# Performance work log

Measured on AMD Instinct MI355X. Metric: run time of the kernel, lower is better.

Reference implementation:

```python
import jax, jax.numpy as jnp
import numpy as np

H, F, E = 1024, 2816, 8   # hidden_size, intermediate_size, num_local_experts
B, S = 2, 2048
TOP_K = 2


def setup_inputs() -> dict:
    key = jax.random.key(0)
    ks = jax.random.split(key, 5)
    scale = 0.02
    return {
        "hidden_states": jax.random.normal(ks[0], (B, S, H), jnp.float32),
        "gate_w": jax.random.normal(ks[1], (E, H), jnp.float32) * scale,
        "w1": jax.random.normal(ks[2], (E, F, H), jnp.float32) * scale,
        "w3": jax.random.normal(ks[3], (E, F, H), jnp.float32) * scale,
        "w2": jax.random.normal(ks[4], (E, H, F), jnp.float32) * scale,
    }


def reference(hidden_states, gate_w, w1, w3, w2):
    b, s, h = hidden_states.shape
    e = gate_w.shape[0]
    T = b * s
    x = hidden_states.reshape(T, h)                      # [T, H]
    router_logits = x @ gate_w.T                         # [T, E]
    probs = jax.nn.softmax(router_logits, axis=-1)
    topw, sel = jax.lax.top_k(probs, TOP_K)              # [T, K]
    topw = topw / jnp.sum(topw, axis=-1, keepdims=True)  # renormalize over top-k
    # dense combine weights [T, E] (equivalent to the per-expert scatter/index_add)
    comb = jnp.zeros((T, e), x.dtype).at[jnp.arange(T)[:, None], sel].add(topw)
    hidden = jax.nn.silu(jnp.einsum('th,efh->etf', x, w1)) * jnp.einsum('th,efh->etf', x, w3)
    y = jnp.einsum('etf,ehf->eth', hidden, w2)           # [E, T, H]
    out = jnp.einsum('eth,te->th', y, comb)              # weighted scatter-combine
    return out.reshape(b, s, h), router_logits
```

## Files before the change

### kernel.cpp

```cpp
#include <hip/hip_runtime.h>
#include <hip/hip_bf16.h>
#include <stdint.h>

#define T_TOK 4096
#define H_DIM 1024
#define F_DIM 2816
#define E_NUM 8

typedef __attribute__((ext_vector_type(8))) __bf16 bf16x8;
typedef __attribute__((ext_vector_type(4))) float floatx4;
typedef __attribute__((address_space(3))) char lds_char;
typedef __attribute__((address_space(1))) const char glb_char;

__device__ __forceinline__ void gload16(const void* g, void* l) {
  __builtin_amdgcn_global_load_lds((glb_char*)g, (lds_char*)l, 16, 0, 0);
}

__device__ __forceinline__ unsigned pack2bf16(float a, float b) {
  unsigned ua = __builtin_bit_cast(unsigned, a);
  unsigned ub = __builtin_bit_cast(unsigned, b);
  ua += 0x7fffu + ((ua >> 16) & 1u);
  ub += 0x7fffu + ((ub >> 16) & 1u);
  return (ua >> 16) | (ub & 0xffff0000u);
}

__device__ __forceinline__ int swz(int row, int colb) {
  return (row * 128 + colb) ^ ((row & 7) << 4);
}

__global__ __launch_bounds__(256) void convert_kernel(
    const float* __restrict__ src, __hip_bfloat16* __restrict__ dst,
    int nchunk8) {
  int i = blockIdx.x * blockDim.x + threadIdx.x;
  const int stride = gridDim.x * blockDim.x;
  for (; i < nchunk8; i += stride) {
    const float4* s = (const float4*)(src + (size_t)i * 8);
    float4 a = s[0], b = s[1];
    uint4 p;
    p.x = pack2bf16(a.x, a.y); p.y = pack2bf16(a.z, a.w);
    p.z = pack2bf16(b.x, b.y); p.w = pack2bf16(b.z, b.w);
    *(uint4*)((char*)dst + (size_t)i * 16) = p;
  }
}

__global__ __launch_bounds__(256) void router_kernel(
    const float* __restrict__ x, const float* __restrict__ gate,
    float* __restrict__ logits_out, __hip_bfloat16* __restrict__ xb,
    int* __restrict__ counts, int* __restrict__ idx_list,
    float* __restrict__ wgt_list)
{
  const int wv = threadIdx.x >> 6;
  const int lane = threadIdx.x & 63;
  const int t = blockIdx.x * 4 + wv;

  const float4* xr = (const float4*)(x + (size_t)t * H_DIM);
  const float4* g4 = (const float4*)gate;

  float acc[E_NUM];
#pragma unroll
  for (int e = 0; e < E_NUM; ++e) acc[e] = 0.f;

  unsigned* xbo = (unsigned*)(xb + (size_t)t * H_DIM);
#pragma unroll
  for (int j = 0; j < 4; ++j) {
    int i = j * 64 + lane;
    float4 xv = xr[i];
    uint2 pk;
    pk.x = pack2bf16(xv.x, xv.y);
    pk.y = pack2bf16(xv.z, xv.w);
    *(uint2*)(xbo + i * 2) = pk;
#pragma unroll
    for (int e = 0; e < E_NUM; ++e) {
      float4 gv = g4[e * 256 + i];
      acc[e] += xv.x * gv.x + xv.y * gv.y + xv.z * gv.z + xv.w * gv.w;
    }
  }
#pragma unroll
  for (int off = 32; off > 0; off >>= 1) {
#pragma unroll
    for (int e = 0; e < E_NUM; ++e) acc[e] += __shfl_xor(acc[e], off, 64);
  }

  if (lane == 0) {
#pragma unroll
    for (int e = 0; e < E_NUM; ++e) logits_out[(size_t)t * E_NUM + e] = acc[e];
    int i0 = 0; float v0 = acc[0];
#pragma unroll
    for (int e = 1; e < E_NUM; ++e) if (acc[e] > v0) { v0 = acc[e]; i0 = e; }
    int i1 = -1; float v1 = -1e30f;
#pragma unroll
    for (int e = 0; e < E_NUM; ++e)
      if (e != i0 && acc[e] > v1) { v1 = acc[e]; i1 = e; }
    float p1 = __expf(v1 - v0);
    float w0 = 1.f / (1.f + p1);
    float w1 = p1 / (1.f + p1);
    int pos0 = atomicAdd(&counts[i0], 1);
    idx_list[i0 * T_TOK + pos0] = t;
    wgt_list[i0 * T_TOK + pos0] = w0;
    int pos1 = atomicAdd(&counts[i1], 1);
    idx_list[i1 * T_TOK + pos1] = t;
    wgt_list[i1 * T_TOK + pos1] = w1;
  }
}

__global__ void scan_kernel(const int* __restrict__ counts,
                            int* __restrict__ offsets) {
  if (threadIdx.x == 0) {
    int s = 0;
    for (int e = 0; e < E_NUM; ++e) { offsets[e] = s; s += counts[e]; }
  }
}

__global__ __launch_bounds__(256) void gemm1_kernel(
    const __hip_bfloat16* __restrict__ xb,
    const __hip_bfloat16* __restrict__ w1b,
    const __hip_bfloat16* __restrict__ w3b,
    const int* __restrict__ counts, const int* __restrict__ offsets,
    const int* __restrict__ idx_list, __hip_bfloat16* __restrict__ hidden)
{
  const int e = blockIdx.z;
  const int n_e = counts[e];
  const int tm = blockIdx.y;
  if (n_e == 0 || tm * 128 >= n_e) return;
  const int tn = blockIdx.x;
  const int f0 = tn * 128;
  const int off_e = offsets[e];

  __shared__ char sA[16384];
  __shared__ char sB1[16384];
  __shared__ char sB3[16384];

  const int tid = threadIdx.x;
  const int lane = tid & 63;
  const int wv = tid >> 6;
  const int wrow = (wv >> 1) * 64;
  const int wcol = (wv & 1) * 64;
  const int csw = ((lane & 7) ^ (lane >> 3)) * 16;
  const int rsub = lane >> 3;

  const char* xbp = (const char*)xb;
  size_t arow[4];
#pragma unroll
  for (int i = 0; i < 4; ++i) {
    int r = wv * 32 + i * 8 + rsub;
    int pos = tm * 128 + r;
    int p = pos < n_e ? pos : n_e - 1;
    arow[i] = (size_t)idx_list[e * T_TOK + p] * (H_DIM * 2);
  }
  const char* w1p = (const char*)w1b + ((size_t)e * F_DIM + f0) * (H_DIM * 2);
  const char* w3p = (const char*)w3b + ((size_t)e * F_DIM + f0) * (H_DIM * 2);

  floatx4 acc1[4][4], acc3[4][4];
#pragma unroll
  for (int m = 0; m < 4; ++m)
#pragma unroll
    for (int n = 0; n < 4; ++n)
#pragma unroll
      for (int r = 0; r < 4; ++r) { acc1[m][n][r] = 0.f; acc3[m][n][r] = 0.f; }

  for (int kt = 0; kt < H_DIM / 64; ++kt) {
    const int kb = kt * 128;
    __syncthreads();
#pragma unroll
    for (int i = 0; i < 4; ++i) {
      int r = wv * 32 + i * 8 + rsub;
      int ldsoff = wv * 4096 + i * 1024;
      gload16(xbp + arow[i] + kb + csw, sA + ldsoff);
      gload16(w1p + (size_t)r * (H_DIM * 2) + kb + csw, sB1 + ldsoff);
      gload16(w3p + (size_t)r * (H_DIM * 2) + kb + csw, sB3 + ldsoff);
    }
    asm volatile("s_waitcnt vmcnt(0)" ::: "memory");
    __syncthreads();
#pragma unroll
    for (int kk = 0; kk < 2; ++kk) {
      const int colb = kk * 64 + (lane >> 4) * 16;
      bf16x8 af[4], bf1[4], bf3[4];
#pragma unroll
      for (int m = 0; m < 4; ++m)
        af[m] = *(const bf16x8*)(sA + swz(wrow + m * 16 + (lane & 15), colb));
#pragma unroll
      for (int n = 0; n < 4; ++n) {
        bf1[n] = *(const bf16x8*)(sB1 + swz(wcol + n * 16 + (lane & 15), colb));
        bf3[n] = *(const bf16x8*)(sB3 + swz(wcol + n * 16 + (lane & 15), colb));
      }
#pragma unroll
      for (int m = 0; m < 4; ++m)
#pragma unroll
        for (int n = 0; n < 4; ++n) {
          acc1[m][n] = __builtin_amdgcn_mfma_f32_16x16x32_bf16(
              af[m], bf1[n], acc1[m][n], 0, 0, 0);
          acc3[m][n] = __builtin_amdgcn_mfma_f32_16x16x32_bf16(
              af[m], bf3[n], acc3[m][n], 0, 0, 0);
        }
    }
  }

#pragma unroll
  for (int m = 0; m < 4; ++m) {
#pragma unroll
    for (int r = 0; r < 4; ++r) {
      int rl = wrow + m * 16 + ((lane >> 4) << 2) + r;
      int pos = tm * 128 + rl;
      if (pos < n_e) {
        __hip_bfloat16* hrow = hidden + (size_t)(off_e + pos) * F_DIM + f0;
#pragma unroll
        for (int n = 0; n < 4; ++n) {
          float h1 = acc1[m][n][r];
          float h3 = acc3[m][n][r];
          float h = (h1 / (1.f + __expf(-h1))) * h3;
          hrow[wcol + n * 16 + (lane & 15)] = __float2bfloat16(h);
        }
      }
    }
  }
}

__global__ __launch_bounds__(256) void gemm2_kernel(
    const __hip_bfloat16* __restrict__ hidden,
    const __hip_bfloat16* __restrict__ w2b,
    const int* __restrict__ counts, const int* __restrict__ offsets,
    const int* __restrict__ idx_list, const float* __restrict__ wgt_list,
    float* __restrict__ out)
{
  const int e = blockIdx.z;
  const int n_e = counts[e];
  const int tm = blockIdx.y;
  if (n_e == 0 || tm * 128 >= n_e) return;
  const int tn = blockIdx.x;
  const int n0 = tn * 128;
  const int off_e = offsets[e];

  __shared__ short sA[128 * 64];
  __shared__ short sB[128 * 64];
  __shared__ int s_tok[128];
  __shared__ float s_wgt[128];

  const int tid = threadIdx.x;
  if (tid < 128) {
    int pos = tm * 128 + tid;
    if (pos < n_e) {
      s_tok[tid] = idx_list[e * T_TOK + pos];
      s_wgt[tid] = wgt_list[e * T_TOK + pos];
    } else {
      s_tok[tid] = -1;
      s_wgt[tid] = 0.f;
    }
  }
  const int lane = tid & 63;
  const int wv = tid >> 6;
  const int wrow = (wv >> 1) * 64;
  const int wcol = (wv & 1) * 64;
  const int cc = tid & 7;
  const int rbase = tid >> 3;

  floatx4 acc[4][4];
#pragma unroll
  for (int m = 0; m < 4; ++m)
#pragma unroll
    for (int n = 0; n < 4; ++n)
#pragma unroll
      for (int r = 0; r < 4; ++r) acc[m][n][r] = 0.f;

  const __hip_bfloat16* w2e = w2b + ((size_t)e * H_DIM + n0) * F_DIM;

  for (int kt = 0; kt < F_DIM / 64; ++kt) {
    const int k0 = kt * 64;
    __syncthreads();
#pragma unroll
    for (int i = 0; i < 4; ++i) {
      int r = rbase + 32 * i;
      int pos = tm * 128 + r;
      int pr = pos < n_e ? pos : n_e - 1;
      uint4 av = *(const uint4*)(hidden + (size_t)(off_e + pr) * F_DIM +
                                 k0 + cc * 8);
      *(uint4*)((char*)sA + swz(r, cc * 16)) = av;
      uint4 bv = *(const uint4*)(w2e + (size_t)r * F_DIM + k0 + cc * 8);
      *(uint4*)((char*)sB + swz(r, cc * 16)) = bv;
    }
    __syncthreads();
#pragma unroll
    for (int kk = 0; kk < 2; ++kk) {
      const int colb = kk * 64 + (lane >> 4) * 16;
      bf16x8 af[4], bf[4];
#pragma unroll
      for (int m = 0; m < 4; ++m)
        af[m] = *(const bf16x8*)((const char*)sA +
                                 swz(wrow + m * 16 + (lane & 15), colb));
#pragma unroll
      for (int n = 0; n < 4; ++n)
        bf[n] = *(const bf16x8*)((const char*)sB +
                                 swz(wcol + n * 16 + (lane & 15), colb));
#pragma unroll
      for (int m = 0; m < 4; ++m)
#pragma unroll
        for (int n = 0; n < 4; ++n)
          acc[m][n] = __builtin_amdgcn_mfma_f32_16x16x32_bf16(
              af[m], bf[n], acc[m][n], 0, 0, 0);
    }
  }

#pragma unroll
  for (int m = 0; m < 4; ++m) {
#pragma unroll
    for (int r = 0; r < 4; ++r) {
      int rl = wrow + m * 16 + ((lane >> 4) << 2) + r;
      int tok = s_tok[rl];
      if (tok >= 0) {
        float wgt = s_wgt[rl];
        float* orow = out + (size_t)tok * H_DIM + n0;
#pragma unroll
        for (int n = 0; n < 4; ++n)
          atomicAdd(&orow[wcol + n * 16 + (lane & 15)], wgt * acc[m][n][r]);
      }
    }
  }
}

__global__ __launch_bounds__(256) void gemm1_fb(
    const __hip_bfloat16* __restrict__ xb,
    const float* __restrict__ w1, const float* __restrict__ w3,
    const int* __restrict__ counts, const int* __restrict__ offsets,
    const int* __restrict__ idx_list, __hip_bfloat16* __restrict__ hidden)
{
  const int e = blockIdx.z;
  const int n_e = counts[e];
  const int tm = blockIdx.y;
  if (n_e == 0 || tm * 128 >= n_e) return;
  const int tn = blockIdx.x;
  const int f0 = tn * 128;
  const int off_e = offsets[e];

  __shared__ short sA[128 * 64];
  __shared__ short sB1[128 * 64];
  __shared__ short sB3[128 * 64];
  __shared__ int s_row[128];

  const int tid = threadIdx.x;
  if (tid < 128) {
    int pos = tm * 128 + tid;
    int p = pos < n_e ? pos : n_e - 1;
    s_row[tid] = idx_list[e * T_TOK + p];
  }
  const int lane = tid & 63;
  const int wv = tid >> 6;
  const int wrow = (wv >> 1) * 64;
  const int wcol = (wv & 1) * 64;
  const int cc = tid & 7;
  const int rbase = tid >> 3;

  floatx4 acc1[4][4], acc3[4][4];
#pragma unroll
  for (int m = 0; m < 4; ++m)
#pragma unroll
    for (int n = 0; n < 4; ++n)
#pragma unroll
      for (int r = 0; r < 4; ++r) { acc1[m][n][r] = 0.f; acc3[m][n][r] = 0.f; }

  const float* w1e = w1 + (size_t)e * F_DIM * H_DIM + (size_t)f0 * H_DIM;
  const float* w3e = w3 + (size_t)e * F_DIM * H_DIM + (size_t)f0 * H_DIM;

  for (int kt = 0; kt < H_DIM / 64; ++kt) {
    const int k0 = kt * 64;
    __syncthreads();
#pragma unroll
    for (int i = 0; i < 4; ++i) {
      int r = rbase + 32 * i;
      uint4 av = *(const uint4*)(xb + (size_t)s_row[r] * H_DIM + k0 + cc * 8);
      *(uint4*)((char*)sA + swz(r, cc * 16)) = av;
      const float4* p1 = (const float4*)(w1e + (size_t)r * H_DIM + k0 + cc * 8);
      float4 a1 = p1[0], b1 = p1[1];
      uint4 pb1;
      pb1.x = pack2bf16(a1.x, a1.y); pb1.y = pack2bf16(a1.z, a1.w);
      pb1.z = pack2bf16(b1.x, b1.y); pb1.w = pack2bf16(b1.z, b1.w);
      *(uint4*)((char*)sB1 + swz(r, cc * 16)) = pb1;
      const float4* p3 = (const float4*)(w3e + (size_t)r * H_DIM + k0 + cc * 8);
      float4 a3 = p3[0], b3 = p3[1];
      uint4 pb3;
      pb3.x = pack2bf16(a3.x, a3.y); pb3.y = pack2bf16(a3.z, a3.w);
      pb3.z = pack2bf16(b3.x, b3.y); pb3.w = pack2bf16(b3.z, b3.w);
      *(uint4*)((char*)sB3 + swz(r, cc * 16)) = pb3;
    }
    __syncthreads();
#pragma unroll
    for (int kk = 0; kk < 2; ++kk) {
      const int colb = kk * 64 + (lane >> 4) * 16;
      bf16x8 af[4], bf1[4], bf3[4];
#pragma unroll
      for (int m = 0; m < 4; ++m)
        af[m] = *(const bf16x8*)((const char*)sA +
                                 swz(wrow + m * 16 + (lane & 15), colb));
#pragma unroll
      for (int n = 0; n < 4; ++n) {
        bf1[n] = *(const bf16x8*)((const char*)sB1 +
                                  swz(wcol + n * 16 + (lane & 15), colb));
        bf3[n] = *(const bf16x8*)((const char*)sB3 +
                                  swz(wcol + n * 16 + (lane & 15), colb));
      }
#pragma unroll
      for (int m = 0; m < 4; ++m)
#pragma unroll
        for (int n = 0; n < 4; ++n) {
          acc1[m][n] = __builtin_amdgcn_mfma_f32_16x16x32_bf16(
              af[m], bf1[n], acc1[m][n], 0, 0, 0);
          acc3[m][n] = __builtin_amdgcn_mfma_f32_16x16x32_bf16(
              af[m], bf3[n], acc3[m][n], 0, 0, 0);
        }
    }
  }
#pragma unroll
  for (int m = 0; m < 4; ++m) {
#pragma unroll
    for (int r = 0; r < 4; ++r) {
      int rl = wrow + m * 16 + ((lane >> 4) << 2) + r;
      int pos = tm * 128 + rl;
      if (pos < n_e) {
        __hip_bfloat16* hrow = hidden + (size_t)(off_e + pos) * F_DIM + f0;
#pragma unroll
        for (int n = 0; n < 4; ++n) {
          float h1 = acc1[m][n][r];
          float h3 = acc3[m][n][r];
          float h = (h1 / (1.f + __expf(-h1))) * h3;
          hrow[wcol + n * 16 + (lane & 15)] = __float2bfloat16(h);
        }
      }
    }
  }
}

__global__ __launch_bounds__(256) void gemm2_fb(
    const __hip_bfloat16* __restrict__ hidden, const float* __restrict__ w2,
    const int* __restrict__ counts, const int* __restrict__ offsets,
    const int* __restrict__ idx_list, const float* __restrict__ wgt_list,
    float* __restrict__ out)
{
  const int e = blockIdx.z;
  const int n_e = counts[e];
  const int tm = blockIdx.y;
  if (n_e == 0 || tm * 128 >= n_e) return;
  const int tn = blockIdx.x;
  const int n0 = tn * 128;
  const int off_e = offsets[e];

  __shared__ short sA[128 * 64];
  __shared__ short sB[128 * 64];
  __shared__ int s_tok[128];
  __shared__ float s_wgt[128];

  const int tid = threadIdx.x;
  if (tid < 128) {
    int pos = tm * 128 + tid;
    if (pos < n_e) {
      s_tok[tid] = idx_list[e * T_TOK + pos];
      s_wgt[tid] = wgt_list[e * T_TOK + pos];
    } else {
      s_tok[tid] = -1;
      s_wgt[tid] = 0.f;
    }
  }
  const int lane = tid & 63;
  const int wv = tid >> 6;
  const int wrow = (wv >> 1) * 64;
  const int wcol = (wv & 1) * 64;
  const int cc = tid & 7;
  const int rbase = tid >> 3;

  floatx4 acc[4][4];
#pragma unroll
  for (int m = 0; m < 4; ++m)
#pragma unroll
    for (int n = 0; n < 4; ++n)
#pragma unroll
      for (int r = 0; r < 4; ++r) acc[m][n][r] = 0.f;

  const float* w2e = w2 + (size_t)e * H_DIM * F_DIM + (size_t)n0 * F_DIM;

  for (int kt = 0; kt < F_DIM / 64; ++kt) {
    const int k0 = kt * 64;
    __syncthreads();
#pragma unroll
    for (int i = 0; i < 4; ++i) {
      int r = rbase + 32 * i;
      int pos = tm * 128 + r;
      int pr = pos < n_e ? pos : n_e - 1;
      uint4 av = *(const uint4*)(hidden + (size_t)(off_e + pr) * F_DIM +
                                 k0 + cc * 8);
      *(uint4*)((char*)sA + swz(r, cc * 16)) = av;
      const float4* pb = (const float4*)(w2e + (size_t)r * F_DIM + k0 + cc * 8);
      float4 ba = pb[0], bb = pb[1];
      uint4 pk;
      pk.x = pack2bf16(ba.x, ba.y); pk.y = pack2bf16(ba.z, ba.w);
      pk.z = pack2bf16(bb.x, bb.y); pk.w = pack2bf16(bb.z, bb.w);
      *(uint4*)((char*)sB + swz(r, cc * 16)) = pk;
    }
    __syncthreads();
#pragma unroll
    for (int kk = 0; kk < 2; ++kk) {
      const int colb = kk * 64 + (lane >> 4) * 16;
      bf16x8 af[4], bf[4];
#pragma unroll
      for (int m = 0; m < 4; ++m)
        af[m] = *(const bf16x8*)((const char*)sA +
                                 swz(wrow + m * 16 + (lane & 15), colb));
#pragma unroll
      for (int n = 0; n < 4; ++n)
        bf[n] = *(const bf16x8*)((const char*)sB +
                                 swz(wcol + n * 16 + (lane & 15), colb));
#pragma unroll
      for (int m = 0; m < 4; ++m)
#pragma unroll
        for (int n = 0; n < 4; ++n)
          acc[m][n] = __builtin_amdgcn_mfma_f32_16x16x32_bf16(
              af[m], bf[n], acc[m][n], 0, 0, 0);
    }
  }
#pragma unroll
  for (int m = 0; m < 4; ++m) {
#pragma unroll
    for (int r = 0; r < 4; ++r) {
      int rl = wrow + m * 16 + ((lane >> 4) << 2) + r;
      int tok = s_tok[rl];
      if (tok >= 0) {
        float wgt = s_wgt[rl];
        float* orow = out + (size_t)tok * H_DIM + n0;
#pragma unroll
        for (int n = 0; n < 4; ++n)
          atomicAdd(&orow[wcol + n * 16 + (lane & 15)], wgt * acc[m][n][r]);
      }
    }
  }
}

extern "C" void kernel_launch(void* const* d_in, const int* in_sizes, int n_in,
                              void* d_out, int out_size, void* d_ws,
                              size_t ws_size, hipStream_t stream) {
  const float* x = (const float*)d_in[0];
  const float* gate = (const float*)d_in[1];
  const float* w1 = (const float*)d_in[2];
  const float* w3 = (const float*)d_in[3];
  const float* w2 = (const float*)d_in[4];

  float* out = (float*)d_out;
  float* logits = out + (size_t)T_TOK * H_DIM;

  char* ws = (char*)d_ws;
  const size_t WEB = (size_t)E_NUM * F_DIM * H_DIM * 2;
  const size_t o_idx = 256;
  const size_t o_wgt = o_idx + (size_t)E_NUM * T_TOK * 4;
  const size_t o_xb  = o_wgt + (size_t)E_NUM * T_TOK * 4;
  const size_t o_hid = o_xb + (size_t)T_TOK * H_DIM * 2;
  const size_t o_w1b = o_hid + (size_t)2 * T_TOK * F_DIM * 2;
  const size_t o_w3b = o_w1b + WEB;
  const size_t o_w2b = o_w3b + WEB;
  const size_t need  = o_w2b + WEB;

  int* counts = (int*)ws;
  int* offsets = counts + 8;
  int* idx_list = (int*)(ws + o_idx);
  float* wgt_list = (float*)(ws + o_wgt);
  __hip_bfloat16* xb = (__hip_bfloat16*)(ws + o_xb);
  __hip_bfloat16* hidden = (__hip_bfloat16*)(ws + o_hid);

  hipMemsetAsync(counts, 0, 64, stream);
  hipMemsetAsync(out, 0, (size_t)T_TOK * H_DIM * sizeof(float), stream);

  if (ws_size >= need) {
    __hip_bfloat16* w1b = (__hip_bfloat16*)(ws + o_w1b);
    __hip_bfloat16* w3b = (__hip_bfloat16*)(ws + o_w3b);
    __hip_bfloat16* w2b = (__hip_bfloat16*)(ws + o_w2b);

    const int NCH = E_NUM * F_DIM * H_DIM / 8;
    convert_kernel<<<2048, 256, 0, stream>>>(w1, w1b, NCH);
    convert_kernel<<<2048, 256, 0, stream>>>(w3, w3b, NCH);
    convert_kernel<<<2048, 256, 0, stream>>>(w2, w2b, NCH);
    router_kernel<<<T_TOK / 4, 256, 0, stream>>>(x, gate, logits, xb, counts,
                                                 idx_list, wgt_list);
    scan_kernel<<<1, 64, 0, stream>>>(counts, offsets);
    gemm1_kernel<<<dim3(F_DIM / 128, T_TOK / 128, E_NUM), 256, 0, stream>>>(
        xb, w1b, w3b, counts, offsets, idx_list, hidden);
    gemm2_kernel<<<dim3(H_DIM / 128, T_TOK / 128, E_NUM), 256, 0, stream>>>(
        hidden, w2b, counts, offsets, idx_list, wgt_list, out);
  } else {
    router_kernel<<<T_TOK / 4, 256, 0, stream>>>(x, gate, logits, xb, counts,
                                                 idx_list, wgt_list);
    scan_kernel<<<1, 64, 0, stream>>>(counts, offsets);
    gemm1_fb<<<dim3(F_DIM / 128, T_TOK / 128, E_NUM), 256, 0, stream>>>(
        xb, w1, w3, counts, offsets, idx_list, hidden);
    gemm2_fb<<<dim3(H_DIM / 128, T_TOK / 128, E_NUM), 256, 0, stream>>>(
        hidden, w2, counts, offsets, idx_list, wgt_list, out);
  }
}
```

Measured before the change: 517.4 us.

## Double-buffer LDS tiles with async global_load_lds in both expert GEMMs

Both grouped GEMM kernels now stage 32-wide K tiles into two LDS buffers and prefetch the next tile with global_load_lds while computing the current one, waiting with partial vmcnt. gemm2 switches from register-staged uint4 loads with LDS stores to direct global-to-LDS loads. A new 4-chunk XOR swizzle matches the narrower tiles. The aim is to hide global load latency behind MFMA work, at the cost of twice as many loop iterations and two barriers per iteration.

Result: slower. 541.2 us (+4.6%).

```diff
diff --git a/kernel.cpp b/kernel.cpp
--- a/kernel.cpp
+++ b/kernel.cpp
@@ -126,29 +126,32 @@
   const int f0 = tn * 128;
   const int off_e = offsets[e];
 
-  __shared__ char sA[16384];
-  __shared__ char sB1[16384];
-  __shared__ char sB3[16384];
+  __shared__ char lds[49152];
+  char* sA  = lds;
+  char* sB1 = lds + 16384;
+  char* sB3 = lds + 32768;
 
   const int tid = threadIdx.x;
   const int lane = tid & 63;
   const int wv = tid >> 6;
   const int wrow = (wv >> 1) * 64;
   const int wcol = (wv & 1) * 64;
-  const int csw = ((lane & 7) ^ (lane >> 3)) * 16;
-  const int rsub = lane >> 3;
-
+
+  const int csw = ((lane & 3) ^ ((lane >> 2) & 3)) << 4;
+  const int r0 = wv * 16 + (lane >> 2);
+  const int r1 = r0 + 64;
+  const int l0 = wv * 1024;
+  const int l1 = wv * 1024 + 4096;
+
+  int p0 = tm * 128 + r0; p0 = p0 < n_e ? p0 : n_e - 1;
+  int p1 = tm * 128 + r1; p1 = p1 < n_e ? p1 : n_e - 1;
+  const size_t arow0 = (size_t)idx_list[e * T_TOK + p0] * 2048;
+  const size_t arow1 = (size_t)idx_list[e * T_TOK + p1] * 2048;
   const char* xbp = (const char*)xb;
-  size_t arow[4];
-#pragma unroll
-  for (int i = 0; i < 4; ++i) {
-    int r = wv * 32 + i * 8 + rsub;
-    int pos = tm * 128 + r;
-    int p = pos < n_e ? pos : n_e - 1;
-    arow[i] = (size_t)idx_list[e * T_TOK + p] * (H_DIM * 2);
-  }
-  const char* w1p = (const char*)w1b + ((size_t)e * F_DIM + f0) * (H_DIM * 2);
-  const char* w3p = (const char*)w3b + ((size_t)e * F_DIM + f0) * (H_DIM * 2);
+  const char* w1p = (const char*)w1b + ((size_t)e * F_DIM + f0) * 2048;
+  const char* w3p = (const char*)w3b + ((size_t)e * F_DIM + f0) * 2048;
+  const size_t b0 = (size_t)r0 * 2048;
+  const size_t b1 = (size_t)r1 * 2048;
 
   floatx4 acc1[4][4], acc3[4][4];
 #pragma unroll
@@ -158,42 +161,58 @@
 #pragma unroll
       for (int r = 0; r < 4; ++r) { acc1[m][n][r] = 0.f; acc3[m][n][r] = 0.f; }
 
-  for (int kt = 0; kt < H_DIM / 64; ++kt) {
-    const int kb = kt * 128;
-    __syncthreads();
-#pragma unroll
-    for (int i = 0; i < 4; ++i) {
-      int r = wv * 32 + i * 8 + rsub;
-      int ldsoff = wv * 4096 + i * 1024;
-      gload16(xbp + arow[i] + kb + csw, sA + ldsoff);
-      gload16(w1p + (size_t)r * (H_DIM * 2) + kb + csw, sB1 + ldsoff);
-      gload16(w3p + (size_t)r * (H_DIM * 2) + kb + csw, sB3 + ldsoff);
-    }
-    asm volatile("s_waitcnt vmcnt(0)" ::: "memory");
-    __syncthreads();
-#pragma unroll
-    for (int kk = 0; kk < 2; ++kk) {
-      const int colb = kk * 64 + (lane >> 4) * 16;
-      bf16x8 af[4], bf1[4], bf3[4];
-#pragma unroll
-      for (int m = 0; m < 4; ++m)
-        af[m] = *(const bf16x8*)(sA + swz(wrow + m * 16 + (lane & 15), colb));
+#define STAGE1(set, kb)                                     \
+  do { char* dA = sA + (set) * 8192;                        \
+       char* dB1 = sB1 + (set) * 8192;                      \
+       char* dB3 = sB3 + (set) * 8192;                      \
+       gload16(xbp + arow0 + (kb) + csw, dA + l0);          \
+       gload16(xbp + arow1 + (kb) + csw, dA + l1);          \
+       gload16(w1p + b0 + (kb) + csw, dB1 + l0);            \
+       gload16(w1p + b1 + (kb) + csw, dB1 + l1);            \
+       gload16(w3p + b0 + (kb) + csw, dB3 + l0);            \
+       gload16(w3p + b1 + (kb) + csw, dB3 + l1); } while (0)
+
+  asm volatile("s_waitcnt vmcnt(0)" ::: "memory");
+  STAGE1(0, 0);
+
+  const int cread = ((lane >> 4) ^ (lane & 3)) << 4;
+  const int ard = (wrow + (lane & 15)) * 64 + cread;
+  const int brd = (wcol + (lane & 15)) * 64 + cread;
+
+#pragma unroll 2
+  for (int kt = 0; kt < H_DIM / 32; ++kt) {
+    const int cur = kt & 1;
+    if (kt < H_DIM / 32 - 1) {
+      STAGE1(cur ^ 1, (kt + 1) * 64);
+      asm volatile("s_waitcnt vmcnt(6)" ::: "memory");
+    } else {
+      asm volatile("s_waitcnt vmcnt(0)" ::: "memory");
+    }
+    __syncthreads();
+    const char* rA  = sA  + cur * 8192;
+    const char* rB1 = sB1 + cur * 8192;
+    const char* rB3 = sB3 + cur * 8192;
+    bf16x8 af[4], bx1[4], bx3[4];
+#pragma unroll
+    for (int m = 0; m < 4; ++m)
+      af[m] = *(const bf16x8*)(rA + ard + m * 1024);
+#pragma unroll
+    for (int n = 0; n < 4; ++n) {
+      bx1[n] = *(const bf16x8*)(rB1 + brd + n * 1024);
+      bx3[n] = *(const bf16x8*)(rB3 + brd + n * 1024);
+    }
+#pragma unroll
+    for (int m = 0; m < 4; ++m)
 #pragma unroll
       for (int n = 0; n < 4; ++n) {
-        bf1[n] = *(const bf16x8*)(sB1 + swz(wcol + n * 16 + (lane & 15), colb));
-        bf3[n] = *(const bf16x8*)(sB3 + swz(wcol + n * 16 + (lane & 15), colb));
+        acc1[m][n] = __builtin_amdgcn_mfma_f32_16x16x32_bf16(
+            af[m], bx1[n], acc1[m][n], 0, 0, 0);
+        acc3[m][n] = __builtin_amdgcn_mfma_f32_16x16x32_bf16(
+            af[m], bx3[n], acc3[m][n], 0, 0, 0);
       }
-#pragma unroll
-      for (int m = 0; m < 4; ++m)
-#pragma unroll
-        for (int n = 0; n < 4; ++n) {
-          acc1[m][n] = __builtin_amdgcn_mfma_f32_16x16x32_bf16(
-              af[m], bf1[n], acc1[m][n], 0, 0, 0);
-          acc3[m][n] = __builtin_amdgcn_mfma_f32_16x16x32_bf16(
-              af[m], bf3[n], acc3[m][n], 0, 0, 0);
-        }
-    }
-  }
+    __syncthreads();
+  }
+#undef STAGE1
 
 #pragma unroll
   for (int m = 0; m < 4; ++m) {
@@ -230,8 +249,9 @@
   const int n0 = tn * 128;
   const int off_e = offsets[e];
 
-  __shared__ short sA[128 * 64];
-  __shared__ short sB[128 * 64];
+  __shared__ char lds[32768];
+  char* sA = lds;
+  char* sB = lds + 16384;
   __shared__ int s_tok[128];
   __shared__ float s_wgt[128];
 
@@ -246,12 +266,26 @@
       s_wgt[tid] = 0.f;
     }
   }
+
   const int lane = tid & 63;
   const int wv = tid >> 6;
   const int wrow = (wv >> 1) * 64;
   const int wcol = (wv & 1) * 64;
-  const int cc = tid & 7;
-  const int rbase = tid >> 3;
+
+  const int csw = ((lane & 3) ^ ((lane >> 2) & 3)) << 4;
+  const int r0 = wv * 16 + (lane >> 2);
+  const int r1 = r0 + 64;
+  const int l0 = wv * 1024;
+  const int l1 = wv * 1024 + 4096;
+
+  int p0 = tm * 128 + r0; p0 = p0 < n_e ? p0 : n_e - 1;
+  int p1 = tm * 128 + r1; p1 = p1 < n_e ? p1 : n_e - 1;
+  const size_t arow0 = (size_t)(off_e + p0) * (F_DIM * 2);
+  const size_t arow1 = (size_t)(off_e + p1) * (F_DIM * 2);
+  const char* hp = (const char*)hidden;
+  const char* w2p = (const char*)w2b + ((size_t)e * H_DIM + n0) * (F_DIM * 2);
+  const size_t b0 = (size_t)r0 * (F_DIM * 2);
+  const size_t b1 = (size_t)r1 * (F_DIM * 2);
 
   floatx4 acc[4][4];
 #pragma unroll
@@ -261,43 +295,49 @@
 #pragma unroll
       for (int r = 0; r < 4; ++r) acc[m][n][r] = 0.f;
 
-  const __hip_bfloat16* w2e = w2b + ((size_t)e * H_DIM + n0) * F_DIM;
-
-  for (int kt = 0; kt < F_DIM / 64; ++kt) {
-    const int k0 = kt * 64;
-    __syncthreads();
-#pragma unroll
-    for (int i = 0; i < 4; ++i) {
-      int r = rbase + 32 * i;
-      int pos = tm * 128 + r;
-      int pr = pos < n_e ? pos : n_e - 1;
-      uint4 av = *(const uint4*)(hidden + (size_t)(off_e + pr) * F_DIM +
-                                 k0 + cc * 8);
-      *(uint4*)((char*)sA + swz(r, cc * 16)) = av;
-      uint4 bv = *(const uint4*)(w2e + (size_t)r * F_DIM + k0 + cc * 8);
-      *(uint4*)((char*)sB + swz(r, cc * 16)) = bv;
-    }
-    __syncthreads();
-#pragma unroll
-    for (int kk = 0; kk < 2; ++kk) {
-      const int colb = kk * 64 + (lane >> 4) * 16;
-      bf16x8 af[4], bf[4];
-#pragma unroll
-      for (int m = 0; m < 4; ++m)
-        af[m] = *(const bf16x8*)((const char*)sA +
-                                 swz(wrow + m * 16 + (lane & 15), colb));
+#define STAGE2(set, kb)                                     \
+  do { char* dA = sA + (set) * 8192;                        \
+       char* dB = sB + (set) * 8192;                        \
+       gload16(hp + arow0 + (kb) + csw, dA + l0);           \
+       gload16(hp + arow1 + (kb) + csw, dA + l1);           \
+       gload16(w2p + b0 + (kb) + csw, dB + l0);             \
+       gload16(w2p + b1 + (kb) + csw, dB + l1); } while (0)
+
+  asm volatile("s_waitcnt vmcnt(0)" ::: "memory");
+  STAGE2(0, 0);
+
+  const int cread = ((lane >> 4) ^ (lane & 3)) << 4;
+  const int ard = (wrow + (lane & 15)) * 64 + cread;
+  const int brd = (wcol + (lane & 15)) * 64 + cread;
+
+#pragma unroll 2
+  for (int kt = 0; kt < F_DIM / 32; ++kt) {
+    const int cur = kt & 1;
+    if (kt < F_DIM / 32 - 1) {
+      STAGE2(cur ^ 1, (kt + 1) * 64);
+      asm volatile("s_waitcnt vmcnt(4)" ::: "memory");
+    } else {
+      asm volatile("s_waitcnt vmcnt(0)" ::: "memory");
+    }
+    __syncthreads();
+    const char* rA = sA + cur * 8192;
+    const char* rB = sB + cur * 8192;
+    bf16x8 af[4], bx[4];
+#pragma unroll
+    for (int m = 0; m < 4; ++m)
+      af[m] = *(const bf16x8*)(rA + ard + m * 1024);
+#pragma unroll
+    for (int n = 0; n < 4; ++n)
+      bx[n] = *(const bf16x8*)(rB + brd + n * 1024);
+#pragma unroll
+    for (int m = 0; m < 4; ++m)
 #pragma unroll
       for (int n = 0; n < 4; ++n)
-        bf[n] = *(const bf16x8*)((const char*)sB +
-                                 swz(wcol + n * 16 + (lane & 15), colb));
-#pragma unroll
-      for (int m = 0; m < 4; ++m)
-#pragma unroll
-        for (int n = 0; n < 4; ++n)
-          acc[m][n] = __builtin_amdgcn_mfma_f32_16x16x32_bf16(
-              af[m], bf[n], acc[m][n], 0, 0, 0);
-    }
-  }
+        acc[m][n] = __builtin_amdgcn_mfma_f32_16x16x32_bf16(
+            af[m], bx[n], acc[m][n], 0, 0, 0);
+    __syncthreads();
+  }
+#undef STAGE2
 
 #pragma unroll
   for (int m = 0; m < 4; ++m) {
```
